# Optimization experiments

Measured on AMD Instinct MI355X. Metric: run time of the kernel, lower is better.

The kernel has to match this reference:

```python
import jax, jax.numpy as jnp
import numpy as np

N_SQ = 64        # number of superquadric primitives
N_PTS = 262144   # number of query points
MIN_E, MAX_E = 0.1, 1.9
TRUNC = 0.1
EPS = 1e-6


def quat2mat(q):
    # q: [4] = (w, x, y, z); normalized before conversion (standard quat2mat)
    q = q / jnp.linalg.norm(q)
    w, x, y, z = q[0], q[1], q[2], q[3]
    return jnp.stack([
        jnp.stack([1.0 - 2.0 * (y * y + z * z), 2.0 * (x * y - w * z), 2.0 * (x * z + w * y)]),
        jnp.stack([2.0 * (x * y + w * z), 1.0 - 2.0 * (x * x + z * z), 2.0 * (y * z - w * x)]),
        jnp.stack([2.0 * (x * z - w * y), 2.0 * (y * z + w * x), 1.0 - 2.0 * (x * x + y * y)]),
    ])


def sdf_point(p, R, t, scale, exps):
    # p: [3] single point; R: [3,3]; t, scale: [3]; exps: [2]
    Xc = R.T @ (p - t)
    sgn = jnp.where(Xc > 0, 1.0, -1.0)          # (x>0)*2-1
    X = sgn * jnp.maximum(jnp.abs(Xc), EPS)
    x, y, z = X[0], X[1], X[2]
    e1, e2 = exps[0], exps[1]
    sx, sy, sz = scale[0], scale[1], scale[2]
    r0 = jnp.sqrt(x * x + y * y + z * z)
    t1 = ((x / sx) ** 2) ** (1.0 / e2)
    t2 = ((y / sy) ** 2) ** (1.0 / e2)
    t3 = ((z / sz) ** 2) ** (1.0 / e1)
    f = ((t1 + t2 + EPS) ** (e2 / e1) + t3) ** (-e1 / 2.0)
    return r0 * (1.0 - f)


def forward_core(raw_scale, raw_exponents, raw_rotation, translation, points):
    scale = jnp.exp(raw_scale)                                        # [N,3]
    exps = jax.nn.sigmoid(raw_exponents) * (MAX_E - MIN_E) + MIN_E    # [N,2]
    R = jax.vmap(quat2mat)(raw_rotation)                              # [N,3,3]
    # value_and_grad wrt the point reproduces torch.autograd.grad normals
    vg_pts = jax.vmap(jax.value_and_grad(sdf_point), in_axes=(0, None, None, None, None))
    vg = jax.vmap(vg_pts, in_axes=(None, 0, 0, 0, 0))
    sdf_all, g = vg(points, R, translation, scale, exps)              # [N,P], [N,P,3]
    nrm = jnp.linalg.norm(g, axis=-1, keepdims=True)
    normals_all = g / jnp.maximum(nrm, 1e-12)                         # F.normalize
    sdf_all = jnp.clip(sdf_all, -TRUNC, TRUNC)                        # truncation before the min-reduce
    idx = jnp.argmin(sdf_all, axis=0)
    sdf = jnp.take_along_axis(sdf_all, idx[None, :], axis=0)[0]       # [P]
    normals = jnp.take_along_axis(normals_all, idx[None, :, None], axis=0)[0]  # [P,3]
    return sdf, normals


def setup_inputs() -> dict:
    key = jax.random.key(0)
    ks = jax.random.split(key, 5)
    return {
        "raw_scale": jax.random.normal(ks[0], (N_SQ, 3), dtype=jnp.float32) * 0.5,
        "raw_exponents": jax.random.normal(ks[1], (N_SQ, 2), dtype=jnp.float32),
        "raw_rotation": jax.random.normal(ks[2], (N_SQ, 4), dtype=jnp.float32),
        "translation": jax.random.normal(ks[3], (N_SQ, 3), dtype=jnp.float32),
        "points": jax.random.normal(ks[4], (N_PTS, 3), dtype=jnp.float32),
    }


def reference(raw_scale, raw_exponents, raw_rotation, translation, points):
    return forward_core(raw_scale, raw_exponents, raw_rotation, translation, points)
```

## Files before the change

kernel.cpp:

```cpp
#include <hip/hip_runtime.h>
#include <math.h>

#define N_SQ 64
#define TRUNCF 0.1f
#define EPSF 1e-6f
#define PTS_PER_BLOCK 128

__device__ __forceinline__ float flog2(float x) { return __builtin_amdgcn_logf(x); }
__device__ __forceinline__ float fexp2(float x) { return __builtin_amdgcn_exp2f(x); }
__device__ __forceinline__ float frcp(float x)  { return __builtin_amdgcn_rcpf(x); }
__device__ __forceinline__ float frsq(float x)  { return __builtin_amdgcn_rsqf(x); }

__global__ __launch_bounds__(64) void prep_kernel(
    const float* __restrict__ raw_scale,
    const float* __restrict__ raw_exp,
    const float* __restrict__ raw_rot,
    const float* __restrict__ trans,
    float4* __restrict__ params)
{
    const int j = threadIdx.x;
    if (j >= N_SQ) return;
    float qw = raw_rot[j * 4 + 0], qx = raw_rot[j * 4 + 1];
    float qy = raw_rot[j * 4 + 2], qz = raw_rot[j * 4 + 3];
    const float qn = sqrtf(qw * qw + qx * qx + qy * qy + qz * qz);
    qw /= qn; qx /= qn; qy /= qn; qz /= qn;
    const float e1 = 1.f / (1.f + expf(-raw_exp[j * 2 + 0])) * 1.8f + 0.1f;
    const float e2 = 1.f / (1.f + expf(-raw_exp[j * 2 + 1])) * 1.8f + 0.1f;
    const float R00 = 1.f - 2.f * (qy * qy + qz * qz);
    const float R01 = 2.f * (qx * qy - qw * qz);
    const float R02 = 2.f * (qx * qz + qw * qy);
    const float R10 = 2.f * (qx * qy + qw * qz);
    const float R11 = 1.f - 2.f * (qx * qx + qz * qz);
    const float R12 = 2.f * (qy * qz - qw * qx);
    const float R20 = 2.f * (qx * qz - qw * qy);
    const float R21 = 2.f * (qy * qz + qw * qx);
    const float R22 = 1.f - 2.f * (qx * qx + qy * qy);
    const float T0 = trans[j * 3 + 0];
    const float T1 = trans[j * 3 + 1];
    const float T2 = trans[j * 3 + 2];
    const float d0 = -(R00 * T0 + R10 * T1 + R20 * T2);
    const float d1 = -(R01 * T0 + R11 * T1 + R21 * T2);
    const float d2 = -(R02 * T0 + R12 * T1 + R22 * T2);
    params[j * 5 + 0] = make_float4(R00, R01, R02, d0);
    params[j * 5 + 1] = make_float4(R10, R11, R12, d1);
    params[j * 5 + 2] = make_float4(R20, R21, R22, d2);
    params[j * 5 + 3] = make_float4(expf(-raw_scale[j * 3 + 0]),
                                    expf(-raw_scale[j * 3 + 1]),
                                    expf(-raw_scale[j * 3 + 2]),
                                    2.f / e2);
    params[j * 5 + 4] = make_float4(2.f / e1, e2 / e1, -e1 * 0.5f, 0.f);
}

__device__ __forceinline__ void write_winner(
    const float4* __restrict__ params,
    float px, float py, float pz, int jb, float best,
    float* __restrict__ out_sdf, float* __restrict__ out_nrm, int p)
{
    const float4 r0v = params[jb * 5 + 0];
    const float4 r1v = params[jb * 5 + 1];
    const float4 r2v = params[jb * 5 + 2];
    const float4 sc  = params[jb * 5 + 3];
    const float4 ex  = params[jb * 5 + 4];

    const float X0 = r0v.x * px + r1v.x * py + r2v.x * pz + r0v.w;
    const float X1 = r0v.y * px + r1v.y * py + r2v.y * pz + r1v.w;
    const float X2 = r0v.z * px + r1v.z * py + r2v.z * pz + r2v.w;

    const float a0 = fabsf(X0), a1 = fabsf(X1), a2 = fabsf(X2);
    const float ax = fmaxf(a0, EPSF);
    const float ay = fmaxf(a1, EPSF);
    const float az = fmaxf(a2, EPSF);
    const float sm0 = (a0 > EPSF) ? ((X0 > 0.f) ? 1.f : -1.f) : 0.f;
    const float sm1 = (a1 > EPSF) ? ((X1 > 0.f) ? 1.f : -1.f) : 0.f;
    const float sm2 = (a2 > EPSF) ? ((X2 > 0.f) ? 1.f : -1.f) : 0.f;

    const float r2 = ax * ax + ay * ay + az * az;
    const float inv_r0 = frsq(r2);
    const float r0 = r2 * inv_r0;

    const float t1 = fexp2(sc.w * flog2(ax * sc.x));
    const float t2 = fexp2(sc.w * flog2(ay * sc.y));
    const float t3 = fexp2(ex.x * flog2(az * sc.z));

    const float A = t1 + t2 + EPSF;
    const float B = fexp2(ex.y * flog2(A));
    const float S = B + t3;
    const float f = fexp2(ex.z * flog2(S));

    const float omf = 1.f - f;
    const float c1  = omf * inv_r0;
    const float w   = r0 * f * frcp(S);
    const float wBA = w * B * frcp(A);

    const float gmx = fmaf(wBA * t1, frcp(ax), c1 * ax);
    const float gmy = fmaf(wBA * t2, frcp(ay), c1 * ay);
    const float gmz = fmaf(w  * t3, frcp(az), c1 * az);
    const float gx = gmx * sm0;
    const float gy = gmy * sm1;
    const float gz = gmz * sm2;
    const float gpx = r0v.x * gx + r0v.y * gy + r0v.z * gz;
    const float gpy = r1v.x * gx + r1v.y * gy + r1v.z * gz;
    const float gpz = r2v.x * gx + r2v.y * gy + r2v.z * gz;

    const float n2 = gpx * gpx + gpy * gpy + gpz * gpz;
    const float inv_n = frsq(fmaxf(n2, 1e-24f));

    out_sdf[p] = best;
    out_nrm[p * 3 + 0] = gpx * inv_n;
    out_nrm[p * 3 + 1] = gpy * inv_n;
    out_nrm[p * 3 + 2] = gpz * inv_n;
}

__device__ __forceinline__ float sdf_eval(
    const float4& r0v, const float4& r1v, const float4& r2v,
    const float4& sc, const float4& ex,
    float px, float py, float pz)
{
    const float X0 = r0v.x * px + r1v.x * py + r2v.x * pz + r0v.w;
    const float X1 = r0v.y * px + r1v.y * py + r2v.y * pz + r1v.w;
    const float X2 = r0v.z * px + r1v.z * py + r2v.z * pz + r2v.w;

    const float ax = fmaxf(fabsf(X0), EPSF);
    const float ay = fmaxf(fabsf(X1), EPSF);
    const float az = fmaxf(fabsf(X2), EPSF);

    const float r2 = ax * ax + ay * ay + az * az;
    const float inv_r0 = frsq(r2);
    const float r0 = r2 * inv_r0;

    const float t1 = fexp2(sc.w * flog2(ax * sc.x));
    const float t2 = fexp2(sc.w * flog2(ay * sc.y));
    const float t3 = fexp2(ex.x * flog2(az * sc.z));

    const float A = t1 + t2 + EPSF;
    const float B = fexp2(ex.y * flog2(A));
    const float S = B + t3;
    const float f = fexp2(ex.z * flog2(S));

    return fminf(fmaxf(r0 * (1.f - f), -TRUNCF), TRUNCF);
}

__global__ __launch_bounds__(256, 8) void superq_main(
    const float4* __restrict__ params,
    const float* __restrict__ points,
    float* __restrict__ out_sdf,
    float* __restrict__ out_nrm,
    int n_pts)
{
    __shared__ float sBest[256];
    __shared__ int   sJb[256];

    const int tid  = threadIdx.x;
    const int lid  = tid & (PTS_PER_BLOCK - 1);
    const int half = tid >> 7;
    const int p    = blockIdx.x * PTS_PER_BLOCK + lid;
    const bool valid = p < n_pts;

    float px = 0.f, py = 0.f, pz = 0.f;
    if (valid) {
        px = points[p * 3 + 0];
        py = points[p * 3 + 1];
        pz = points[p * 3 + 2];
    }

    const int j0 = __builtin_amdgcn_readfirstlane(half * (N_SQ / 2));
    const float4* __restrict__ Pb = params + j0 * 5;

    float best = INFINITY;
    int jb = j0;

    float4 c00 = Pb[0], c01 = Pb[1], c02 = Pb[2], c03 = Pb[3], c04 = Pb[4];
    float4 c10 = Pb[5], c11 = Pb[6], c12 = Pb[7], c13 = Pb[8], c14 = Pb[9];

    for (int jj = 0; jj < N_SQ / 2; jj += 2) {
        const float4* Pn = Pb + (jj + 2) * 5;
        const float4 n00 = Pn[0], n01 = Pn[1], n02 = Pn[2], n03 = Pn[3], n04 = Pn[4];
        const float4 n10 = Pn[5], n11 = Pn[6], n12 = Pn[7], n13 = Pn[8], n14 = Pn[9];

        const float s0 = sdf_eval(c00, c01, c02, c03, c04, px, py, pz);
        const float s1 = sdf_eval(c10, c11, c12, c13, c14, px, py, pz);

        const bool t0 = s0 < best;
        best = t0 ? s0 : best;
        jb   = t0 ? (j0 + jj) : jb;
        const bool t1 = s1 < best;
        best = t1 ? s1 : best;
        jb   = t1 ? (j0 + jj + 1) : jb;

        c00 = n00; c01 = n01; c02 = n02; c03 = n03; c04 = n04;
        c10 = n10; c11 = n11; c12 = n12; c13 = n13; c14 = n14;
    }

    sBest[tid] = best;
    sJb[tid]   = jb;
    __syncthreads();

    if (tid < PTS_PER_BLOCK && valid) {
        const float bl = sBest[tid];
        const float bh = sBest[tid + PTS_PER_BLOCK];
        const int   jl = sJb[tid];
        const int   jh = sJb[tid + PTS_PER_BLOCK];
        const bool hi_wins = bh < bl;
        const float bw = hi_wins ? bh : bl;
        const int   jw = hi_wins ? jh : jl;
        write_winner(params, px, py, pz, jw, bw, out_sdf, out_nrm, p);
    }
}

extern "C" void kernel_launch(void* const* d_in, const int* in_sizes, int n_in,
                              void* d_out, int out_size, void* d_ws, size_t ws_size,
                              hipStream_t stream) {
    const float* raw_scale = (const float*)d_in[0];
    const float* raw_exp   = (const float*)d_in[1];
    const float* raw_rot   = (const float*)d_in[2];
    const float* trans     = (const float*)d_in[3];
    const float* points    = (const float*)d_in[4];
    float* out = (float*)d_out;

    const int n_pts = in_sizes[4] / 3;
    float* out_sdf = out;
    float* out_nrm = out + n_pts;

    float4* params = (float4*)d_ws;

    prep_kernel<<<1, 64, 0, stream>>>(raw_scale, raw_exp, raw_rot, trans, params);

    const int grid = (n_pts + PTS_PER_BLOCK - 1) / PTS_PER_BLOCK;
    superq_main<<<grid, 256, 0, stream>>>(params, points, out_sdf, out_nrm, n_pts);
}
```

Baseline: 93.41 us.

## Pack two points per lane with v2f math and split primitives across four waves

Each lane now evaluates two points at once as float2 vectors, so the compiler can emit packed FP32 instructions (v_pk_fma/v_pk_mul) for the transform and polynomial math. Primitives are split across four waves of 16 each instead of two halves of 32, with a four-way shared-memory argmin reduction. Transcendentals stay scalar, and the winner pass reloads point coordinates from global memory. The aim is to cut VALU instruction count per point, at the cost of more registers and a larger reduction.

```diff
diff --git a/kernel.cpp b/kernel.cpp
--- a/kernel.cpp
+++ b/kernel.cpp
@@ -6,10 +6,20 @@
 #define EPSF 1e-6f
 #define PTS_PER_BLOCK 128
 
+typedef float v2f __attribute__((ext_vector_type(2)));
+
 __device__ __forceinline__ float flog2(float x) { return __builtin_amdgcn_logf(x); }
 __device__ __forceinline__ float fexp2(float x) { return __builtin_amdgcn_exp2f(x); }
 __device__ __forceinline__ float frcp(float x)  { return __builtin_amdgcn_rcpf(x); }
 __device__ __forceinline__ float frsq(float x)  { return __builtin_amdgcn_rsqf(x); }
+
+__device__ __forceinline__ v2f splat(float s) { v2f r; r.x = s; r.y = s; return r; }
+__device__ __forceinline__ v2f vlog2(v2f v) { v2f r; r.x = flog2(v.x); r.y = flog2(v.y); return r; }
+__device__ __forceinline__ v2f vexp2(v2f v) { v2f r; r.x = fexp2(v.x); r.y = fexp2(v.y); return r; }
+__device__ __forceinline__ v2f vrsq (v2f v) { v2f r; r.x = frsq(v.x);  r.y = frsq(v.y);  return r; }
+__device__ __forceinline__ v2f vmax2(v2f a, v2f b) { return __builtin_elementwise_max(a, b); }
+__device__ __forceinline__ v2f vmin2(v2f a, v2f b) { return __builtin_elementwise_min(a, b); }
+__device__ __forceinline__ v2f vabs2(v2f a) { return __builtin_elementwise_abs(a); }
 
 __global__ __launch_bounds__(64) void prep_kernel(
     const float* __restrict__ raw_scale,
@@ -111,35 +121,6 @@
     out_nrm[p * 3 + 2] = gpz * inv_n;
 }
 
-__device__ __forceinline__ float sdf_eval(
-    const float4& r0v, const float4& r1v, const float4& r2v,
-    const float4& sc, const float4& ex,
-    float px, float py, float pz)
-{
-    const float X0 = r0v.x * px + r1v.x * py + r2v.x * pz + r0v.w;
-    const float X1 = r0v.y * px + r1v.y * py + r2v.y * pz + r1v.w;
-    const float X2 = r0v.z * px + r1v.z * py + r2v.z * pz + r2v.w;
-
-    const float ax = fmaxf(fabsf(X0), EPSF);
-    const float ay = fmaxf(fabsf(X1), EPSF);
-    const float az = fmaxf(fabsf(X2), EPSF);
-
-    const float r2 = ax * ax + ay * ay + az * az;
-    const float inv_r0 = frsq(r2);
-    const float r0 = r2 * inv_r0;
-
-    const float t1 = fexp2(sc.w * flog2(ax * sc.x));
-    const float t2 = fexp2(sc.w * flog2(ay * sc.y));
-    const float t3 = fexp2(ex.x * flog2(az * sc.z));
-
-    const float A = t1 + t2 + EPSF;
-    const float B = fexp2(ex.y * flog2(A));
-    const float S = B + t3;
-    const float f = fexp2(ex.z * flog2(S));
-
-    return fminf(fmaxf(r0 * (1.f - f), -TRUNCF), TRUNCF);
-}
-
 __global__ __launch_bounds__(256, 8) void superq_main(
     const float4* __restrict__ params,
     const float* __restrict__ points,
@@ -147,63 +128,99 @@
     float* __restrict__ out_nrm,
     int n_pts)
 {
-    __shared__ float sBest[256];
-    __shared__ int   sJb[256];
+    __shared__ float sBest[4][PTS_PER_BLOCK];
+    __shared__ int   sJb[4][PTS_PER_BLOCK];
 
     const int tid  = threadIdx.x;
-    const int lid  = tid & (PTS_PER_BLOCK - 1);
-    const int half = tid >> 7;
-    const int p    = blockIdx.x * PTS_PER_BLOCK + lid;
-    const bool valid = p < n_pts;
-
-    float px = 0.f, py = 0.f, pz = 0.f;
-    if (valid) {
-        px = points[p * 3 + 0];
-        py = points[p * 3 + 1];
-        pz = points[p * 3 + 2];
+    const int lane = tid & 63;
+    const int wave = tid >> 6;
+    const int base = blockIdx.x * PTS_PER_BLOCK;
+    const int q0 = 2 * lane, q1 = q0 + 1;
+    const int pA = base + q0;
+    const int pB = base + q1;
+    const bool vA = pA < n_pts;
+    const bool vB = pB < n_pts;
+
+    v2f px = splat(0.f), py = splat(0.f), pz = splat(0.f);
+    if (vB) {
+        const float2* pv = (const float2*)(points + pA * 3);
+        const float2 v0 = pv[0], v1 = pv[1], v2 = pv[2];
+        px.x = v0.x; py.x = v0.y; pz.x = v1.x;
+        px.y = v1.y; py.y = v2.x; pz.y = v2.y;
+    } else if (vA) {
+        px.x = points[pA * 3 + 0];
+        py.x = points[pA * 3 + 1];
+        pz.x = points[pA * 3 + 2];
     }
 
-    const int j0 = __builtin_amdgcn_readfirstlane(half * (N_SQ / 2));
-    const float4* __restrict__ Pb = params + j0 * 5;
-
-    float best = INFINITY;
-    int jb = j0;
-
-    float4 c00 = Pb[0], c01 = Pb[1], c02 = Pb[2], c03 = Pb[3], c04 = Pb[4];
-    float4 c10 = Pb[5], c11 = Pb[6], c12 = Pb[7], c13 = Pb[8], c14 = Pb[9];
-
-    for (int jj = 0; jj < N_SQ / 2; jj += 2) {
-        const float4* Pn = Pb + (jj + 2) * 5;
-        const float4 n00 = Pn[0], n01 = Pn[1], n02 = Pn[2], n03 = Pn[3], n04 = Pn[4];
-        const float4 n10 = Pn[5], n11 = Pn[6], n12 = Pn[7], n13 = Pn[8], n14 = Pn[9];
-
-        const float s0 = sdf_eval(c00, c01, c02, c03, c04, px, py, pz);
-        const float s1 = sdf_eval(c10, c11, c12, c13, c14, px, py, pz);
-
-        const bool t0 = s0 < best;
-        best = t0 ? s0 : best;
-        jb   = t0 ? (j0 + jj) : jb;
-        const bool t1 = s1 < best;
-        best = t1 ? s1 : best;
-        jb   = t1 ? (j0 + jj + 1) : jb;
-
-        c00 = n00; c01 = n01; c02 = n02; c03 = n03; c04 = n04;
-        c10 = n10; c11 = n11; c12 = n12; c13 = n13; c14 = n14;
+    const int j0 = __builtin_amdgcn_readfirstlane(wave * (N_SQ / 4));
+
+    v2f best = splat(INFINITY);
+    int jbx = j0, jby = j0;
+
+    #pragma unroll 2
+    for (int jj = 0; jj < N_SQ / 4; ++jj) {
+        const int j = j0 + jj;
+        const float4 r0v = params[j * 5 + 0];
+        const float4 r1v = params[j * 5 + 1];
+        const float4 r2v = params[j * 5 + 2];
+        const float4 sc  = params[j * 5 + 3];
+        const float4 ex  = params[j * 5 + 4];
+
+        const v2f X0 = r0v.x * px + r1v.x * py + r2v.x * pz + r0v.w;
+        const v2f X1 = r0v.y * px + r1v.y * py + r2v.y * pz + r1v.w;
+        const v2f X2 = r0v.z * px + r1v.z * py + r2v.z * pz + r2v.w;
+
+        const v2f ax = vmax2(vabs2(X0), splat(EPSF));
+        const v2f ay = vmax2(vabs2(X1), splat(EPSF));
+        const v2f az = vmax2(vabs2(X2), splat(EPSF));
+
+        const v2f r2 = ax * ax + ay * ay + az * az;
+        const v2f inv_r0 = vrsq(r2);
+        const v2f r0 = r2 * inv_r0;
+
+        const v2f t1 = vexp2(sc.w * vlog2(ax * sc.x));
+        const v2f t2 = vexp2(sc.w * vlog2(ay * sc.y));
+        const v2f t3 = vexp2(ex.x * vlog2(az * sc.z));
+
+        const v2f A = t1 + t2 + EPSF;
+        const v2f B = vexp2(ex.y * vlog2(A));
+        const v2f S = B + t3;
+        const v2f f = vexp2(ex.z * vlog2(S));
+
+        const v2f sdf  = r0 * (1.f - f);
+        const v2f sdfc = vmin2(vmax2(sdf, splat(-TRUNCF)), splat(TRUNCF));
+
+        const bool tx = sdfc.x < best.x;
+        best.x = tx ? sdfc.x : best.x;
+        jbx    = tx ? j : jbx;
+        const bool ty = sdfc.y < best.y;
+        best.y = ty ? sdfc.y : best.y;
+        jby    = ty ? j : jby;
     }
 
-    sBest[tid] = best;
-    sJb[tid]   = jb;
+    sBest[wave][q0] = best.x;  sJb[wave][q0] = jbx;
+    sBest[wave][q1] = best.y;  sJb[wave][q1] = jby;
     __syncthreads();
 
-    if (tid < PTS_PER_BLOCK && valid) {
-        const float bl = sBest[tid];
-        const float bh = sBest[tid + PTS_PER_BLOCK];
-        const int   jl = sJb[tid];
-        const int   jh = sJb[tid + PTS_PER_BLOCK];
-        const bool hi_wins = bh < bl;
-        const float bw = hi_wins ? bh : bl;
-        const int   jw = hi_wins ? jh : jl;
-        write_winner(params, px, py, pz, jw, bw, out_sdf, out_nrm, p);
+    if (tid < PTS_PER_BLOCK) {
+        const int p = base + tid;
+        if (p < n_pts) {
+            float bw = sBest[0][tid];
+            int   jw = sJb[0][tid];
+            #pragma unroll
+            for (int w = 1; w < 4; ++w) {
+                const float b  = sBest[w][tid];
+                const int   jj = sJb[w][tid];
+                const bool win = b < bw;
+                bw = win ? b : bw;
+                jw = win ? jj : jw;
+            }
+            const float cx = points[p * 3 + 0];
+            const float cy = points[p * 3 + 1];
+            const float cz = points[p * 3 + 2];
+            write_winner(params, cx, cy, cz, jw, bw, out_sdf, out_nrm, p);
+        }
     }
 }
 
```

Result: faster. 88.12 us (-5.7%).
